# Performance work log

Hardware: AMD Instinct MI355X
Metric: run time of the kernel (lower is better)

## Reference

```python
import jax, jax.numpy as jnp
import numpy as np
from jax import lax

D_MODEL = 1024
D_FF = 4096
NUM_EXPERTS = 24
TOP_K = 2
B, S = 2, 2048


def setup_inputs() -> dict:
    key = jax.random.key(0)
    ks = jax.random.split(key, 5)
    x = jax.random.normal(ks[0], (B, S, D_MODEL), dtype=jnp.float32)
    gate_w = jax.random.normal(ks[1], (D_MODEL, NUM_EXPERTS), dtype=jnp.float32) * 0.02
    gate_b = jnp.zeros((NUM_EXPERTS,), dtype=jnp.float32)
    w1 = jax.random.normal(ks[2], (NUM_EXPERTS, D_MODEL, D_FF), dtype=jnp.float32) * 0.02
    b1 = jnp.zeros((NUM_EXPERTS, D_FF), dtype=jnp.float32)
    w2 = jax.random.normal(ks[3], (NUM_EXPERTS, D_FF, D_MODEL), dtype=jnp.float32) * 0.02
    b2 = jnp.zeros((NUM_EXPERTS, D_MODEL), dtype=jnp.float32)
    return {"x": x, "gate_w": gate_w, "gate_b": gate_b,
            "w1": w1, "b1": b1, "w2": w2, "b2": b2}


def reference(x, gate_w, gate_b, w1, b1, w2, b2):
    b, s, d = x.shape
    t = b * s
    xf = x.reshape(t, d)  # [T, d]
    scores = xf @ gate_w + gate_b  # [T, E]
    top_val, top_idx = lax.top_k(scores, TOP_K)  # [T, k]
    prob = jax.nn.softmax(top_val, axis=-1)  # softmax over the top-k logits
    # scatter top-k probabilities into dense per-expert combine weights [T, E]
    combine = jnp.zeros((t, NUM_EXPERTS), dtype=x.dtype)
    combine = combine.at[jnp.arange(t)[:, None], top_idx].add(prob)

    def body(acc, expert):
        w1e, b1e, w2e, b2e, ce = expert  # ce: [T]
        h = jax.nn.gelu(xf @ w1e + b1e, approximate=False)  # exact GELU as torch default
        y = h @ w2e + b2e  # [T, d]
        return acc + ce[:, None] * y, None

    out, _ = lax.scan(body, jnp.zeros_like(xf), (w1, b1, w2, b2, combine.T))
    return out.reshape(b, s, d)
```

## Files before the change

### kernel.cpp

```cpp
#include <hip/hip_runtime.h>
#include <math.h>

#define DM 1024
#define DF 4096
#define NE 24
#define T_TOK 4096
#define T2 (T_TOK*2)

#define BM 128
#define BN 128
#define BK 64
#define MTILES 8
#define NK1 (DM / BK)
#define NK2 (DF / BK)

typedef __attribute__((ext_vector_type(4))) float f32x4;
typedef __attribute__((ext_vector_type(8))) short s16x8;

static __device__ __forceinline__ unsigned short f2bf(float f) {
    unsigned int u = __float_as_uint(f);
    unsigned int r = u + 0x7fffu + ((u >> 16) & 1u);
    return (unsigned short)(r >> 16);
}

static __device__ __forceinline__ unsigned int cvtpk(float lo, float hi) {
    unsigned int r;
    asm("v_cvt_pk_bf16_f32 %0, %1, %2" : "=v"(r) : "v"(lo), "v"(hi));
    return r;
}

#define GLL(gsrc, ldst)                                                          \
    __builtin_amdgcn_global_load_lds(                                            \
        (const __attribute__((address_space(1))) void*)(gsrc),                   \
        (__attribute__((address_space(3))) void*)(ldst), 16, 0, 0)


__global__ void k_transpose_gw(const float* __restrict__ gw, float* __restrict__ gwT) {
    int e = blockIdx.x;
    for (int d = threadIdx.x; d < DM; d += blockDim.x)
        gwT[e * DM + d] = gw[d * NE + e];
}

__global__ void k_gate(const float* __restrict__ x, const float* __restrict__ gwT,
                       const float* __restrict__ gb,
                       int* __restrict__ idx, float* __restrict__ prob) {
    int wave = threadIdx.x >> 6;
    int lane = threadIdx.x & 63;
    int t = blockIdx.x * 4 + wave;
    if (t >= T_TOK) return;
    const float* xr = x + (size_t)t * DM;
    float acc[NE];
#pragma unroll
    for (int e = 0; e < NE; e++) acc[e] = 0.f;
    for (int i = 0; i < DM / 64; i++) {
        int d = lane + i * 64;
        float xv = xr[d];
#pragma unroll
        for (int e = 0; e < NE; e++) acc[e] = fmaf(xv, gwT[e * DM + d], acc[e]);
    }
#pragma unroll
    for (int e = 0; e < NE; e++) {
        float v = acc[e];
        for (int off = 32; off >= 1; off >>= 1) v += __shfl_xor(v, off);
        acc[e] = v;
    }
    if (lane == 0) {
        float v1 = -1e30f, v2 = -1e30f;
        int i1 = -1, i2 = -1;
        for (int e = 0; e < NE; e++) {
            float s = acc[e] + gb[e];
            if (s > v1) { v2 = v1; i2 = i1; v1 = s; i1 = e; }
            else if (s > v2) { v2 = s; i2 = e; }
        }
        float e2 = expf(v2 - v1);
        float inv = 1.f / (1.f + e2);
        idx[t * 2] = i1; idx[t * 2 + 1] = i2;
        prob[t * 2] = inv; prob[t * 2 + 1] = e2 * inv;
    }
}


__global__ __launch_bounds__(1024)
void k_route(const int* __restrict__ idx, int* __restrict__ counts,
             int* __restrict__ offsets, int* __restrict__ slot_tok,
             int* __restrict__ pair_slot) {
    __shared__ int cnt[NE], offs[NE], cur[NE];
    const int tid = threadIdx.x;
    if (tid < NE) cnt[tid] = 0;
    __syncthreads();
    for (int i = tid; i < T2; i += 1024) atomicAdd(&cnt[idx[i]], 1);
    __syncthreads();
    if (tid == 0) {
        int s = 0;
        for (int e = 0; e < NE; e++) {
            offs[e] = s; offsets[e] = s; counts[e] = cnt[e]; s += cnt[e];
        }
    }
    if (tid < NE) cur[tid] = 0;
    __syncthreads();
    for (int i = tid; i < T2; i += 1024) {
        int e = idx[i];
        int pos = offs[e] + atomicAdd(&cur[e], 1);
        slot_tok[pos] = i >> 1;
        pair_slot[i] = pos;
    }
}

__global__ void k_gather(const float* __restrict__ x, const int* __restrict__ slot_tok,
                         unsigned short* __restrict__ Xg) {
    int s = blockIdx.x;
    int tok = slot_tok[s];
    const float4* src = (const float4*)(x + (size_t)tok * DM);
    ushort4* dst = (ushort4*)(Xg + (size_t)s * DM);
    for (int i = threadIdx.x; i < DM / 4; i += blockDim.x) {
        float4 v = src[i];
        ushort4 o;
        o.x = f2bf(v.x); o.y = f2bf(v.y); o.z = f2bf(v.z); o.w = f2bf(v.w);
        dst[i] = o;
    }
}

__global__ void k_combine(const float* __restrict__ Y, const int* __restrict__ pair_slot,
                          const float* __restrict__ prob, const int* __restrict__ idx,
                          const float* __restrict__ b2, float* __restrict__ out) {
    int t = blockIdx.x;
    int s1 = pair_slot[t * 2], s2 = pair_slot[t * 2 + 1];
    int e1 = idx[t * 2], e2 = idx[t * 2 + 1];
    float p1 = prob[t * 2], p2 = prob[t * 2 + 1];
    const float4* y1 = (const float4*)(Y + (size_t)s1 * DM);
    const float4* y2 = (const float4*)(Y + (size_t)s2 * DM);
    const float4* ba = (const float4*)(b2 + (size_t)e1 * DM);
    const float4* bb = (const float4*)(b2 + (size_t)e2 * DM);
    float4* o = (float4*)(out + (size_t)t * DM);
    int i = threadIdx.x;
    float4 a = y1[i], b = y2[i], c = ba[i], d = bb[i];
    float4 r;
    r.x = p1 * (a.x + c.x) + p2 * (b.x + d.x);
    r.y = p1 * (a.y + c.y) + p2 * (b.y + d.y);
    r.z = p1 * (a.z + c.z) + p2 * (b.z + d.z);
    r.w = p1 * (a.w + c.w) + p2 * (b.w + d.w);
    o[i] = r;
}


__global__ __launch_bounds__(512)
void k_mm1(const unsigned short* __restrict__ Xg, const float* __restrict__ w1,
           const float* __restrict__ b1, const int* __restrict__ counts,
           const int* __restrict__ offsets, unsigned short* __restrict__ H) {
    const int TOT = NE * MTILES * (DF / BN);
    int work = (blockIdx.x & 7) * (TOT >> 3) + (blockIdx.x >> 3);
    const int mt = work % MTILES;
    const int en = work / MTILES;
    const int e  = en >> 5;
    const int n0 = (en & 31) * BN;
    const int ne = counts[e];
    const int m0 = mt * BM;
    if (m0 >= ne) return;
    const int rows = min(BM, ne - m0);
    const int slotbase = offsets[e] + m0;

    __shared__ unsigned short As[BM * BK];
    __shared__ float          Bf[BK * BN];
    __shared__ unsigned short Bs[BN * BK];

    const int tid  = threadIdx.x;
    const int lane = tid & 63;
    const int w    = tid >> 6;
    const int wm   = w >> 1, wn = w & 1;

    const float* w1e = w1 + (size_t)e * DM * DF;
    const int arow = lane >> 3;
    const int gchunk = ((lane & 7) ^ arow) * 8;

    const int swz0 = ((lane >> 4) ^ (lane & 7)) << 4;
    const int swz1 = ((4 | (lane >> 4)) ^ (lane & 7)) << 4;
    const char* Arow = (const char*)As + (wm * 32 + (lane & 15)) * 128;
    const char* Brow = (const char*)Bs + (wn * 64 + (lane & 15)) * 128;

    const int cn = tid & 127;
    const int ck = (tid >> 7) * 16;
    const int cc0 = ((ck >> 3) ^ (cn & 7)) << 4;
    const int cc1 = (((ck >> 3) + 1) ^ (cn & 7)) << 4;
    char* BsRowC = (char*)Bs + cn * 128;

    f32x4 acc[2][4];
#pragma unroll
    for (int a = 0; a < 2; a++)
#pragma unroll
        for (int b = 0; b < 4; b++) acc[a][b] = (f32x4)0.f;

#pragma unroll 1
    for (int kt = 0; kt < NK1; ++kt) {
        const int k0 = kt * BK;
#pragma unroll
        for (int q = 0; q < 2; q++) {
            int row = (w * 2 + q) * 8 + arow;
            GLL(Xg + (size_t)(slotbase + row) * DM + k0 + gchunk,
                &As[(w * 2 + q) * 512]);
        }
#pragma unroll
        for (int q = 0; q < 4; q++) {
            GLL(w1e + (size_t)(k0 + w * 8 + q * 2 + (lane >> 5)) * DF + n0 + (lane & 31) * 4,
                &Bf[(w * 8 + q * 2) * BN]);
        }
        __syncthreads();
        s16x8 af[2][2];
#pragma unroll
        for (int f = 0; f < 2; f++) {
            af[0][f] = *(const s16x8*)(Arow + f * 2048 + swz0);
            af[1][f] = *(const s16x8*)(Arow + f * 2048 + swz1);
        }
        {
            uint4 v0, v1;
            v0.x = cvtpk(Bf[(ck + 0) * BN + cn], Bf[(ck + 1) * BN + cn]);
            v0.y = cvtpk(Bf[(ck + 2) * BN + cn], Bf[(ck + 3) * BN + cn]);
            v0.z = cvtpk(Bf[(ck + 4) * BN + cn], Bf[(ck + 5) * BN + cn]);
            v0.w = cvtpk(Bf[(ck + 6) * BN + cn], Bf[(ck + 7) * BN + cn]);
            v1.x = cvtpk(Bf[(ck + 8) * BN + cn], Bf[(ck + 9) * BN + cn]);
            v1.y = cvtpk(Bf[(ck + 10) * BN + cn], Bf[(ck + 11) * BN + cn]);
            v1.z = cvtpk(Bf[(ck + 12) * BN + cn], Bf[(ck + 13) * BN + cn]);
            v1.w = cvtpk(Bf[(ck + 14) * BN + cn], Bf[(ck + 15) * BN + cn]);
            *(uint4*)(BsRowC + cc0) = v0;
            *(uint4*)(BsRowC + cc1) = v1;
        }
        __syncthreads();
        s16x8 bfr[2][4];
#pragma unroll
        for (int f = 0; f < 4; f++) {
            bfr[0][f] = *(const s16x8*)(Brow + f * 2048 + swz0);
            bfr[1][f] = *(const s16x8*)(Brow + f * 2048 + swz1);
        }
#pragma unroll
        for (int ks = 0; ks < 2; ks++)
#pragma unroll
            for (int fm = 0; fm < 2; fm++)
#pragma unroll
                for (int fn = 0; fn < 4; fn++)
                    acc[fm][fn] = __builtin_amdgcn_mfma_f32_16x16x32_bf16(
                        af[ks][fm], bfr[ks][fn], acc[fm][fn], 0, 0, 0);
        __syncthreads();
    }

    const float* b1e = b1 + (size_t)e * DF;
#pragma unroll
    for (int fm = 0; fm < 2; fm++) {
        const int mrow = wm * 32 + fm * 16 + ((lane >> 4) << 2);
#pragma unroll
        for (int fn = 0; fn < 4; fn++) {
            const int ncol = n0 + wn * 64 + fn * 16 + (lane & 15);
            const float bb = b1e[ncol];
#pragma unroll
            for (int r = 0; r < 4; r++) {
                const int m = mrow + r;
                if (m < rows) {
                    float h = acc[fm][fn][r] + bb;
                    h = 0.5f * h * (1.f + erff(h * 0.70710678118654752f));
                    H[(size_t)(slotbase + m) * DF + ncol] = f2bf(h);
                }
            }
        }
    }
}

__global__ __launch_bounds__(512)
void k_mm2(const unsigned short* __restrict__ Hb, const float* __restrict__ w2,
           const int* __restrict__ counts, const int* __restrict__ offsets,
           float* __restrict__ Y) {
    const int TOT = NE * MTILES * (DM / BN);
    int work = (blockIdx.x & 7) * (TOT >> 3) + (blockIdx.x >> 3);
    const int mt = work % MTILES;
    const int en = work / MTILES;
    const int e  = en >> 3;
    const int n0 = (en & 7) * BN;
    const int ne = counts[e];
    const int m0 = mt * BM;
    if (m0 >= ne) return;
    const int rows = min(BM, ne - m0);
    const int slotbase = offsets[e] + m0;

    __shared__ unsigned short As[BM * BK];
    __shared__ float          Bf[BK * BN];
    __shared__ unsigned short Bs[BN * BK];

    const int tid  = threadIdx.x;
    const int lane = tid & 63;
    const int w    = tid >> 6;
    const int wm   = w >> 1, wn = w & 1;

    const float* w2e = w2 + (size_t)e * DF * DM;
    const int arow = lane >> 3;
    const int gchunk = ((lane & 7) ^ arow) * 8;

    const int swz0 = ((lane >> 4) ^ (lane & 7)) << 4;
    const int swz1 = ((4 | (lane >> 4)) ^ (lane & 7)) << 4;
    const char* Arow = (const char*)As + (wm * 32 + (lane & 15)) * 128;
    const char* Brow = (const char*)Bs + (wn * 64 + (lane & 15)) * 128;

    const int cn = tid & 127;
    const int ck = (tid >> 7) * 16;
    const int cc0 = ((ck >> 3) ^ (cn & 7)) << 4;
    const int cc1 = (((ck >> 3) + 1) ^ (cn & 7)) << 4;
    char* BsRowC = (char*)Bs + cn * 128;

    f32x4 acc[2][4];
#pragma unroll
    for (int a = 0; a < 2; a++)
#pragma unroll
        for (int b = 0; b < 4; b++) acc[a][b] = (f32x4)0.f;

#pragma unroll 1
    for (int kt = 0; kt < NK2; ++kt) {
        const int k0 = kt * BK;
#pragma unroll
        for (int q = 0; q < 2; q++) {
            int row = (w * 2 + q) * 8 + arow;
            GLL(Hb + (size_t)(slotbase + row) * DF + k0 + gchunk,
                &As[(w * 2 + q) * 512]);
        }
#pragma unroll
        for (int q = 0; q < 4; q++) {
            GLL(w2e + (size_t)(k0 + w * 8 + q * 2 + (lane >> 5)) * DM + n0 + (lane & 31) * 4,
                &Bf[(w * 8 + q * 2) * BN]);
        }
        __syncthreads();
        s16x8 af[2][2];
#pragma unroll
        for (int f = 0; f < 2; f++) {
            af[0][f] = *(const s16x8*)(Arow + f * 2048 + swz0);
            af[1][f] = *(const s16x8*)(Arow + f * 2048 + swz1);
        }
        {
            uint4 v0, v1;
            v0.x = cvtpk(Bf[(ck + 0) * BN + cn], Bf[(ck + 1) * BN + cn]);
            v0.y = cvtpk(Bf[(ck + 2) * BN + cn], Bf[(ck + 3) * BN + cn]);
            v0.z = cvtpk(Bf[(ck + 4) * BN + cn], Bf[(ck + 5) * BN + cn]);
            v0.w = cvtpk(Bf[(ck + 6) * BN + cn], Bf[(ck + 7) * BN + cn]);
            v1.x = cvtpk(Bf[(ck + 8) * BN + cn], Bf[(ck + 9) * BN + cn]);
            v1.y = cvtpk(Bf[(ck + 10) * BN + cn], Bf[(ck + 11) * BN + cn]);
            v1.z = cvtpk(Bf[(ck + 12) * BN + cn], Bf[(ck + 13) * BN + cn]);
            v1.w = cvtpk(Bf[(ck + 14) * BN + cn], Bf[(ck + 15) * BN + cn]);
            *(uint4*)(BsRowC + cc0) = v0;
            *(uint4*)(BsRowC + cc1) = v1;
        }
        __syncthreads();
        s16x8 bfr[2][4];
#pragma unroll
        for (int f = 0; f < 4; f++) {
            bfr[0][f] = *(const s16x8*)(Brow + f * 2048 + swz0);
            bfr[1][f] = *(const s16x8*)(Brow + f * 2048 + swz1);
        }
#pragma unroll
        for (int ks = 0; ks < 2; ks++)
#pragma unroll
            for (int fm = 0; fm < 2; fm++)
#pragma unroll
                for (int fn = 0; fn < 4; fn++)
                    acc[fm][fn] = __builtin_amdgcn_mfma_f32_16x16x32_bf16(
                        af[ks][fm], bfr[ks][fn], acc[fm][fn], 0, 0, 0);
        __syncthreads();
    }

#pragma unroll
    for (int fm = 0; fm < 2; fm++) {
        const int mrow = wm * 32 + fm * 16 + ((lane >> 4) << 2);
#pragma unroll
        for (int fn = 0; fn < 4; fn++) {
            const int ncol = n0 + wn * 64 + fn * 16 + (lane & 15);
#pragma unroll
            for (int r = 0; r < 4; r++) {
                const int m = mrow + r;
                if (m < rows)
                    Y[(size_t)(slotbase + m) * DM + ncol] = acc[fm][fn][r];
            }
        }
    }
}


extern "C" void kernel_launch(void* const* d_in, const int* in_sizes, int n_in,
                              void* d_out, int out_size, void* d_ws, size_t ws_size,
                              hipStream_t stream) {
    const float* x   = (const float*)d_in[0];
    const float* gw  = (const float*)d_in[1];
    const float* gb  = (const float*)d_in[2];
    const float* w1  = (const float*)d_in[3];
    const float* b1  = (const float*)d_in[4];
    const float* w2  = (const float*)d_in[5];
    const float* b2  = (const float*)d_in[6];
    float* out = (float*)d_out;

    size_t off = 0;
    auto alloc = [&](size_t bytes) {
        void* p = (char*)d_ws + off;
        off += (bytes + 255) & ~(size_t)255;
        return p;
    };
    float* gwT       = (float*)alloc(NE * DM * sizeof(float));
    int*   idx       = (int*)alloc(T2 * sizeof(int));
    float* prob      = (float*)alloc(T2 * sizeof(float));
    int*   counts    = (int*)alloc(32 * sizeof(int));
    int*   offsets   = (int*)alloc(32 * sizeof(int));
    int*   slot_tok  = (int*)alloc(T2 * sizeof(int));
    int*   pair_slot = (int*)alloc(T2 * sizeof(int));
    unsigned short* Xg = (unsigned short*)alloc((size_t)(T2 + BM) * DM * sizeof(unsigned short));
    unsigned short* Hb = (unsigned short*)alloc((size_t)(T2 + BM) * DF * sizeof(unsigned short));
    float* Yb        = (float*)alloc((size_t)(T2 + BM) * DM * sizeof(float));

    k_transpose_gw<<<NE, 256, 0, stream>>>(gw, gwT);
    k_gate<<<T_TOK / 4, 256, 0, stream>>>(x, gwT, gb, idx, prob);
    k_route<<<1, 1024, 0, stream>>>(idx, counts, offsets, slot_tok, pair_slot);
    k_gather<<<T2, 256, 0, stream>>>(x, slot_tok, Xg);

    k_mm1<<<NE * MTILES * (DF / BN), 512, 0, stream>>>(Xg, w1, b1, counts, offsets, Hb);
    k_mm2<<<NE * MTILES * (DM / BN), 512, 0, stream>>>(Hb, w2, counts, offsets, Yb);
    k_combine<<<T_TOK, 256, 0, stream>>>(Yb, pair_slot, prob, idx, b2, out);
}
```

Measured before the change: 562.4 us.

## Double-buffer A tiles and prefetch fp32 weights into registers for overlap

Both expert GEMM kernels now keep two LDS buffers for the activation tile and load the next k-step's fp32 weight slice into registers while the current step computes. The weights are converted to bf16 from registers and written straight into the swizzled B tile, so the fp32 staging buffer in LDS is no longer needed. The synchronisation is reworked to one full barrier plus a lightweight wait-and-barrier per iteration. This is meant to hide global load latency behind MFMA work. In exchange it uses more registers and relies on subtle barrier and waitcnt ordering for correctness.

```diff
diff --git a/kernel.cpp b/kernel.cpp
--- a/kernel.cpp
+++ b/kernel.cpp
@@ -15,6 +15,7 @@
 #define NK2 (DF / BK)
 
 typedef __attribute__((ext_vector_type(4))) float f32x4;
+typedef __attribute__((ext_vector_type(2))) float f32x2;
 typedef __attribute__((ext_vector_type(8))) short s16x8;
 
 static __device__ __forceinline__ unsigned short f2bf(float f) {
@@ -159,8 +160,7 @@
     const int rows = min(BM, ne - m0);
     const int slotbase = offsets[e] + m0;
 
-    __shared__ unsigned short As[BM * BK];
-    __shared__ float          Bf[BK * BN];
+    __shared__ unsigned short As[2][BM * BK];
     __shared__ unsigned short Bs[BN * BK];
 
     const int tid  = threadIdx.x;
@@ -174,14 +174,14 @@
 
     const int swz0 = ((lane >> 4) ^ (lane & 7)) << 4;
     const int swz1 = ((4 | (lane >> 4)) ^ (lane & 7)) << 4;
-    const char* Arow = (const char*)As + (wm * 32 + (lane & 15)) * 128;
-    const char* Brow = (const char*)Bs + (wn * 64 + (lane & 15)) * 128;
-
-    const int cn = tid & 127;
-    const int ck = (tid >> 7) * 16;
-    const int cc0 = ((ck >> 3) ^ (cn & 7)) << 4;
-    const int cc1 = (((ck >> 3) + 1) ^ (cn & 7)) << 4;
-    char* BsRowC = (char*)Bs + cn * 128;
+    const char* Arow0 = (const char*)As[0] + (wm * 32 + (lane & 15)) * 128;
+    const char* Arow1 = (const char*)As[1] + (wm * 32 + (lane & 15)) * 128;
+    const char* Brow  = (const char*)Bs + (wn * 64 + (lane & 15)) * 128;
+
+    const int np = (tid & 63) * 2;
+    const int ckw = w;
+    char* BsW0 = (char*)Bs + (np + 0) * 128 + ((ckw ^ ((np + 0) & 7)) << 4);
+    char* BsW1 = (char*)Bs + (np + 1) * 128 + ((ckw ^ ((np + 1) & 7)) << 4);
 
     f32x4 acc[2][4];
 #pragma unroll
@@ -189,41 +189,52 @@
 #pragma unroll
         for (int b = 0; b < 4; b++) acc[a][b] = (f32x4)0.f;
 
-#pragma unroll 1
-    for (int kt = 0; kt < NK1; ++kt) {
-        const int k0 = kt * BK;
+    f32x2 L[8];
+    auto loadB = [&](int k0) {
+#pragma unroll
+        for (int j = 0; j < 8; j++)
+            L[j] = *(const f32x2*)(w1e + (size_t)(k0 + w * 8 + j) * DF + n0 + np);
+    };
+    auto stageA = [&](int buf, int k0) {
 #pragma unroll
         for (int q = 0; q < 2; q++) {
             int row = (w * 2 + q) * 8 + arow;
             GLL(Xg + (size_t)(slotbase + row) * DM + k0 + gchunk,
-                &As[(w * 2 + q) * 512]);
-        }
-#pragma unroll
-        for (int q = 0; q < 4; q++) {
-            GLL(w1e + (size_t)(k0 + w * 8 + q * 2 + (lane >> 5)) * DF + n0 + (lane & 31) * 4,
-                &Bf[(w * 8 + q * 2) * BN]);
-        }
+                &As[buf][(w * 2 + q) * 512]);
+        }
+    };
+
+    stageA(0, 0);
+    loadB(0);
+#pragma unroll 1
+    for (int kt = 0; kt < NK1; ++kt) {
+        const int cur = kt & 1;
         __syncthreads();
+        if (kt + 1 < NK1) stageA(cur ^ 1, (kt + 1) * BK);
+        {
+            uint4 v0, v1;
+            v0.x = cvtpk(L[0][0], L[1][0]);
+            v0.y = cvtpk(L[2][0], L[3][0]);
+            v0.z = cvtpk(L[4][0], L[5][0]);
+            v0.w = cvtpk(L[6][0], L[7][0]);
+            v1.x = cvtpk(L[0][1], L[1][1]);
+            v1.y = cvtpk(L[2][1], L[3][1]);
+            v1.z = cvtpk(L[4][1], L[5][1]);
+            v1.w = cvtpk(L[6][1], L[7][1]);
+            *(uint4*)BsW0 = v0;
+            *(uint4*)BsW1 = v1;
+        }
+        if (kt + 1 < NK1) loadB((kt + 1) * BK);
+        const char* Arow = cur ? Arow1 : Arow0;
         s16x8 af[2][2];
 #pragma unroll
         for (int f = 0; f < 2; f++) {
             af[0][f] = *(const s16x8*)(Arow + f * 2048 + swz0);
             af[1][f] = *(const s16x8*)(Arow + f * 2048 + swz1);
         }
-        {
-            uint4 v0, v1;
-            v0.x = cvtpk(Bf[(ck + 0) * BN + cn], Bf[(ck + 1) * BN + cn]);
-            v0.y = cvtpk(Bf[(ck + 2) * BN + cn], Bf[(ck + 3) * BN + cn]);
-            v0.z = cvtpk(Bf[(ck + 4) * BN + cn], Bf[(ck + 5) * BN + cn]);
-            v0.w = cvtpk(Bf[(ck + 6) * BN + cn], Bf[(ck + 7) * BN + cn]);
-            v1.x = cvtpk(Bf[(ck + 8) * BN + cn], Bf[(ck + 9) * BN + cn]);
-            v1.y = cvtpk(Bf[(ck + 10) * BN + cn], Bf[(ck + 11) * BN + cn]);
-            v1.z = cvtpk(Bf[(ck + 12) * BN + cn], Bf[(ck + 13) * BN + cn]);
-            v1.w = cvtpk(Bf[(ck + 14) * BN + cn], Bf[(ck + 15) * BN + cn]);
-            *(uint4*)(BsRowC + cc0) = v0;
-            *(uint4*)(BsRowC + cc1) = v1;
-        }
-        __syncthreads();
+        asm volatile("s_waitcnt lgkmcnt(0)" ::: "memory");
+        __builtin_amdgcn_s_barrier();
+        __builtin_amdgcn_sched_barrier(0);
         s16x8 bfr[2][4];
 #pragma unroll
         for (int f = 0; f < 4; f++) {
@@ -238,7 +249,6 @@
                 for (int fn = 0; fn < 4; fn++)
                     acc[fm][fn] = __builtin_amdgcn_mfma_f32_16x16x32_bf16(
                         af[ks][fm], bfr[ks][fn], acc[fm][fn], 0, 0, 0);
-        __syncthreads();
     }
 
     const float* b1e = b1 + (size_t)e * DF;
@@ -278,8 +288,7 @@
     const int rows = min(BM, ne - m0);
     const int slotbase = offsets[e] + m0;
 
-    __shared__ unsigned short As[BM * BK];
-    __shared__ float          Bf[BK * BN];
+    __shared__ unsigned short As[2][BM * BK];
     __shared__ unsigned short Bs[BN * BK];
 
     const int tid  = threadIdx.x;
@@ -293,14 +302,14 @@
 
     const int swz0 = ((lane >> 4) ^ (lane & 7)) << 4;
     const int swz1 = ((4 | (lane >> 4)) ^ (lane & 7)) << 4;
-    const char* Arow = (const char*)As + (wm * 32 + (lane & 15)) * 128;
-    const char* Brow = (const char*)Bs + (wn * 64 + (lane & 15)) * 128;
-
-    const int cn = tid & 127;
-    const int ck = (tid >> 7) * 16;
-    const int cc0 = ((ck >> 3) ^ (cn & 7)) << 4;
-    const int cc1 = (((ck >> 3) + 1) ^ (cn & 7)) << 4;
-    char* BsRowC = (char*)Bs + cn * 128;
+    const char* Arow0 = (const char*)As[0] + (wm * 32 + (lane & 15)) * 128;
+    const char* Arow1 = (const char*)As[1] + (wm * 32 + (lane & 15)) * 128;
+    const char* Brow  = (const char*)Bs + (wn * 64 + (lane & 15)) * 128;
+
+    const int np = (tid & 63) * 2;
+    const int ckw = w;
+    char* BsW0 = (char*)Bs + (np + 0) * 128 + ((ckw ^ ((np + 0) & 7)) << 4);
+    char* BsW1 = (char*)Bs + (np + 1) * 128 + ((ckw ^ ((np + 1) & 7)) << 4);
 
     f32x4 acc[2][4];
 #pragma unroll
@@ -308,41 +317,52 @@
 #pragma unroll
         for (int b = 0; b < 4; b++) acc[a][b] = (f32x4)0.f;
 
-#pragma unroll 1
-    for (int kt = 0; kt < NK2; ++kt) {
-        const int k0 = kt * BK;
+    f32x2 L[8];
+    auto loadB = [&](int k0) {
+#pragma unroll
+        for (int j = 0; j < 8; j++)
+            L[j] = *(const f32x2*)(w2e + (size_t)(k0 + w * 8 + j) * DM + n0 + np);
+    };
+    auto stageA = [&](int buf, int k0) {
 #pragma unroll
         for (int q = 0; q < 2; q++) {
             int row = (w * 2 + q) * 8 + arow;
             GLL(Hb + (size_t)(slotbase + row) * DF + k0 + gchunk,
-                &As[(w * 2 + q) * 512]);
-        }
-#pragma unroll
-        for (int q = 0; q < 4; q++) {
-            GLL(w2e + (size_t)(k0 + w * 8 + q * 2 + (lane >> 5)) * DM + n0 + (lane & 31) * 4,
-                &Bf[(w * 8 + q * 2) * BN]);
-        }
+                &As[buf][(w * 2 + q) * 512]);
+        }
+    };
+
+    stageA(0, 0);
+    loadB(0);
+#pragma unroll 1
+    for (int kt = 0; kt < NK2; ++kt) {
+        const int cur = kt & 1;
         __syncthreads();
+        if (kt + 1 < NK2) stageA(cur ^ 1, (kt + 1) * BK);
+        {
+            uint4 v0, v1;
+            v0.x = cvtpk(L[0][0], L[1][0]);
+            v0.y = cvtpk(L[2][0], L[3][0]);
+            v0.z = cvtpk(L[4][0], L[5][0]);
+            v0.w = cvtpk(L[6][0], L[7][0]);
+            v1.x = cvtpk(L[0][1], L[1][1]);
+            v1.y = cvtpk(L[2][1], L[3][1]);
+            v1.z = cvtpk(L[4][1], L[5][1]);
+            v1.w = cvtpk(L[6][1], L[7][1]);
+            *(uint4*)BsW0 = v0;
+            *(uint4*)BsW1 = v1;
+        }
+        if (kt + 1 < NK2) loadB((kt + 1) * BK);
+        const char* Arow = cur ? Arow1 : Arow0;
         s16x8 af[2][2];
 #pragma unroll
         for (int f = 0; f < 2; f++) {
             af[0][f] = *(const s16x8*)(Arow + f * 2048 + swz0);
             af[1][f] = *(const s16x8*)(Arow + f * 2048 + swz1);
         }
-        {
-            uint4 v0, v1;
-            v0.x = cvtpk(Bf[(ck + 0) * BN + cn], Bf[(ck + 1) * BN + cn]);
-            v0.y = cvtpk(Bf[(ck + 2) * BN + cn], Bf[(ck + 3) * BN + cn]);
-            v0.z = cvtpk(Bf[(ck + 4) * BN + cn], Bf[(ck + 5) * BN + cn]);
-            v0.w = cvtpk(Bf[(ck + 6) * BN + cn], Bf[(ck + 7) * BN + cn]);
-            v1.x = cvtpk(Bf[(ck + 8) * BN + cn], Bf[(ck + 9) * BN + cn]);
-            v1.y = cvtpk(Bf[(ck + 10) * BN + cn], Bf[(ck + 11) * BN + cn]);
-            v1.z = cvtpk(Bf[(ck + 12) * BN + cn], Bf[(ck + 13) * BN + cn]);
-            v1.w = cvtpk(Bf[(ck + 14) * BN + cn], Bf[(ck + 15) * BN + cn]);
-            *(uint4*)(BsRowC + cc0) = v0;
-            *(uint4*)(BsRowC + cc1) = v1;
-        }
-        __syncthreads();
+        asm volatile("s_waitcnt lgkmcnt(0)" ::: "memory");
+        __builtin_amdgcn_s_barrier();
+        __builtin_amdgcn_sched_barrier(0);
         s16x8 bfr[2][4];
 #pragma unroll
         for (int f = 0; f < 4; f++) {
@@ -357,7 +377,6 @@
                 for (int fn = 0; fn < 4; fn++)
                     acc[fm][fn] = __builtin_amdgcn_mfma_f32_16x16x32_bf16(
                         af[ks][fm], bfr[ks][fn], acc[fm][fn], 0, 0, 0);
-        __syncthreads();
     }
 
 #pragma unroll
```

After: 533.3 us. -5.2%, faster.
